# Performance work log

Hardware: AMD Instinct MI355X
Metric: run time of the kernel (lower is better)

The kernel has to match this reference:

```python
import jax, jax.numpy as jnp
import numpy as np


def setup_inputs() -> dict:
    key = jax.random.key(0)
    k1, k2 = jax.random.split(key)
    B, G, P = 64, 4999, 50
    raw_gene_expr = jax.random.normal(k1, (B, G), dtype=jnp.float32)
    # binary pathway membership matrix, mimics torch.randint(0, 2, (P, G)).float()
    pathway_gene_matrix = (jax.random.uniform(k2, (P, G)) < 0.5).astype(jnp.float32)
    return {"raw_gene_expr": raw_gene_expr, "pathway_gene_matrix": pathway_gene_matrix}


def reference(raw_gene_expr, pathway_gene_matrix):
    """Vectorized ssGSEA enrichment (compute_pathway_activations0).

    raw_gene_expr:        [B, G] float
    pathway_gene_matrix:  [P, G] binary float
    returns:              [B, P] signed max-deviation enrichment scores
    """
    B, G = raw_gene_expr.shape
    P = pathway_gene_matrix.shape[0]

    # Sort genes per sample in descending expression order
    order = jnp.argsort(-raw_gene_expr, axis=1)                      # [B, G]
    sorted_expr = jnp.take_along_axis(raw_gene_expr, order, axis=1)  # [B, G]

    # hit[b, p, i] = 1 if gene at sorted position i belongs to pathway p
    hit = (pathway_gene_matrix[:, order] > 0)                        # [P, B, G]
    hit = jnp.transpose(hit, (1, 0, 2)).astype(raw_gene_expr.dtype)  # [B, P, G]

    size = jnp.sum(pathway_gene_matrix > 0, axis=1).astype(raw_gene_expr.dtype)  # [P]

    # Weighted hit increments: |expr|^0.25 over hits, normalized per (sample, pathway)
    w = (jnp.abs(sorted_expr) ** 0.25)[:, None, :] * hit             # [B, P, G]
    s = jnp.sum(w, axis=-1, keepdims=True)
    w = jnp.where(s > 0, w / jnp.where(s > 0, s, 1.0), w)

    cum_hit = jnp.cumsum(w, axis=-1)                                 # [B, P, G]
    denom = jnp.maximum(G - size, 1.0)[None, :, None]                # guard size==G
    cum_miss = jnp.cumsum((1.0 - hit) / denom, axis=-1)              # [B, P, G]

    running = cum_hit - cum_miss                                     # [B, P, G]
    pos = jnp.argmax(jnp.abs(running), axis=-1)                      # [B, P]
    # signed max deviation == running value at the argmax of |running|
    es = jnp.take_along_axis(running, pos[..., None], axis=-1)[..., 0]  # [B, P]
    es = jnp.where(size[None, :] > 0, es, 0.0)
    return es
```

## Files before the change

kernel.cpp:

```cpp
#include <hip/hip_runtime.h>
#include <math.h>

typedef unsigned long long ull;

constexpr int Bc = 64;
constexpr int Gc = 4999;
constexpr int Pc = 50;

constexpr int RUN   = 1024;
constexpr int NRUN  = 5;
constexpr int NPAD  = NRUN * RUN;
constexpr int LPW   = 79;
constexpr ull PADKEY = 0xFFFFFFFFFFFFFFFFull;

__device__ __forceinline__ ull shfl_xor64(ull v, int lm) {
    int lo = __shfl_xor((int)(unsigned)(v & 0xFFFFFFFFull), lm, 64);
    int hi = __shfl_xor((int)(unsigned)(v >> 32), lm, 64);
    return ((ull)(unsigned)hi << 32) | (unsigned)lo;
}

__global__ __launch_bounds__(256) void chunk_sort(
    const float* __restrict__ expr, const float* __restrict__ pathway,
    ull* __restrict__ runs, ull* __restrict__ pbits, int P, int G)
{
    __shared__ ull key[RUN];
    const int r = blockIdx.x, b = blockIdx.y, tid = threadIdx.x;
    const int base = tid * 4;
    const float* row = expr + (size_t)b * G;

    ull v[4];
#pragma unroll
    for (int o = 0; o < 4; ++o) {
        int i = r * RUN + base + o;
        if (i < G) {
            unsigned u = __float_as_uint(row[i]);
            unsigned m = (u >> 31) ? ~u : (u | 0x80000000u);
            v[o] = ((ull)(~m) << 32) | (unsigned)i;
        } else {
            v[o] = PADKEY;
        }
    }

    for (int kk = 2; kk <= RUN; kk <<= 1) {
        const int j0 = kk >> 1;
        if (j0 >= 256) {
#pragma unroll
            for (int o = 0; o < 4; ++o) key[base + o] = v[o];
            __syncthreads();
            for (int j = j0; j >= 256; j >>= 1) {
#pragma unroll
                for (int t = tid; t < RUN / 2; t += 256) {
                    int i  = ((t & ~(j - 1)) << 1) | (t & (j - 1));
                    int ix = i | j;
                    ull a = key[i], c = key[ix];
                    bool up = ((i & kk) == 0);
                    if ((a > c) == up) { key[i] = c; key[ix] = a; }
                }
                __syncthreads();
            }
#pragma unroll
            for (int o = 0; o < 4; ++o) v[o] = key[base + o];
        }
        int jstart = (j0 > 128) ? 128 : j0;
        for (int j = jstart; j >= 4; j >>= 1) {
            int lm = j >> 2;
            bool takeMin = (((tid & lm) == 0) == ((base & kk) == 0));
#pragma unroll
            for (int o = 0; o < 4; ++o) {
                ull c = shfl_xor64(v[o], lm);
                ull mn = (v[o] < c) ? v[o] : c;
                ull mx = (v[o] < c) ? c : v[o];
                v[o] = takeMin ? mn : mx;
            }
        }
#pragma unroll
        for (int j = 2; j >= 1; j >>= 1) {
            if (j < kk) {
#pragma unroll
                for (int o = 0; o < 4; ++o) {
                    if ((o & j) == 0) {
                        bool up = (((base + o) & kk) == 0);
                        ull a = v[o], c = v[o | j];
                        if ((a > c) == up) { v[o] = c; v[o | j] = a; }
                    }
                }
            }
        }
    }

    ull* dst = runs + ((size_t)b * NRUN + r) * RUN;
#pragma unroll
    for (int o = 0; o < 4; ++o) dst[base + o] = v[o];

    if (r == 0) {
        int g = b * 256 + tid;
        if (g < G) {
            ull m = 0;
#pragma unroll
            for (int p = 0; p < Pc; ++p)
                if (pathway[(size_t)p * G + g] > 0.0f) m |= (1ull << p);
            pbits[g] = m;
        }
    }
}

__global__ __launch_bounds__(1024) void rank_scatter(
    const ull* __restrict__ runs,
    float* __restrict__ wqout, unsigned short* __restrict__ sidxout, int G)
{
    __shared__ ull runsLDS[NPAD];
    const int rg = blockIdx.x, b = blockIdx.y, tid = threadIdx.x;

    const ull* rowruns = runs + (size_t)b * NPAD;
    for (int i = tid; i < NPAD; i += 1024) runsLDS[i] = rowruns[i];
    __syncthreads();

    const int e = rg * 1024 + tid;
    const ull keyv = runsLDS[e];
    if (keyv == PADKEY) return;

    const int run = e >> 10;
    int rank = e & 1023;
#pragma unroll
    for (int rr = 0; rr < NRUN; ++rr) {
        if (rr == run) continue;
        const ull* arr = &runsLDS[rr * RUN];
        int pos = 0;
#pragma unroll
        for (int s = RUN; s >= 1; s >>= 1) {
            int np = pos + s;
            if (np <= RUN && arr[np - 1] < keyv) pos = np;
        }
        rank += pos;
    }

    int idx = (int)(unsigned)(keyv & 0xFFFFFFFFu);
    unsigned m = ~((unsigned)(keyv >> 32));
    unsigned absbits = ((m >> 31) ? m : ~m) & 0x7FFFFFFFu;
    float av = __uint_as_float(absbits);
    wqout[(size_t)b * G + rank] = sqrtf(sqrtf(av));
    sidxout[(size_t)b * G + rank] = (unsigned short)idx;
}

__global__ __launch_bounds__(256) void es_kernel(
    const float* __restrict__ wq, const unsigned short* __restrict__ sidx,
    const ull* __restrict__ pbits, float* __restrict__ out, int B, int P, int G)
{
    __shared__ float    swq[Gc];
    __shared__ unsigned sm32[Gc];

    const int pg = blockIdx.x;
    const int b  = blockIdx.y;
    const int tid = threadIdx.x;
    const int pbeg = pg * 13;
    const int pend = (pbeg + 13 < P) ? (pbeg + 13) : P;

    for (int i = tid; i < G; i += 256) {
        swq[i]  = wq[(size_t)b * G + i];
        sm32[i] = (unsigned)(pbits[sidx[(size_t)b * G + i]] >> pbeg);
    }
    __syncthreads();

    const int lane = tid & 63;
    const int w = tid >> 6;
    const int p0 = pbeg + w * 4;
    if (p0 >= pend) return;
    const int sh4 = w * 4;

    const int start = lane * LPW;
    const int cnt = (start + LPW < G) ? LPW : (G - start);

    double sw[4] = {0.0, 0.0, 0.0, 0.0};
    int sh[4] = {0, 0, 0, 0};
    for (int k = 0; k < cnt; ++k) {
        int s = start + k;
        unsigned nib = (sm32[s] >> sh4) & 15u;
        double wv = (double)swq[s];
#pragma unroll
        for (int q = 0; q < 4; ++q) {
            if ((nib >> q) & 1u) { sw[q] += wv; sh[q]++; }
        }
    }
    double norm[4], inv_denom[4], running[4];
    int sht[4];
#pragma unroll
    for (int q = 0; q < 4; ++q) {
        double swt = sw[q];
        int shq = sh[q];
#pragma unroll
        for (int off = 1; off < 64; off <<= 1) {
            swt += __shfl_xor(swt, off, 64);
            shq += __shfl_xor(shq, off, 64);
        }
        sht[q] = shq;
        norm[q]      = (swt > 0.0) ? 1.0 / swt : 1.0;
        inv_denom[q] = 1.0 / fmax((double)(G - shq), 1.0);
        double csum = sw[q] * norm[q] - (double)(cnt - sh[q]) * inv_denom[q];
        double x = csum;
#pragma unroll
        for (int off = 1; off < 64; off <<= 1) {
            double vv = __shfl_up(x, off, 64);
            if (lane >= off) x += vv;
        }
        running[q] = x - csum;
    }

    double bestv[4] = {-1.0, -1.0, -1.0, -1.0};
    double bestr[4] = {0.0, 0.0, 0.0, 0.0};
    int besti[4] = {0x7FFFFFFF, 0x7FFFFFFF, 0x7FFFFFFF, 0x7FFFFFFF};
    for (int k = 0; k < cnt; ++k) {
        int s = start + k;
        unsigned nib = (sm32[s] >> sh4) & 15u;
        double wv = (double)swq[s];
#pragma unroll
        for (int q = 0; q < 4; ++q) {
            running[q] += ((nib >> q) & 1u) ? wv * norm[q] : -inv_denom[q];
            double a = fabs(running[q]);
            if (a > bestv[q]) { bestv[q] = a; bestr[q] = running[q]; besti[q] = s; }
        }
    }
#pragma unroll
    for (int q = 0; q < 4; ++q) {
#pragma unroll
        for (int off = 1; off < 64; off <<= 1) {
            double ov  = __shfl_xor(bestv[q], off, 64);
            double orr = __shfl_xor(bestr[q], off, 64);
            int    oi  = __shfl_xor(besti[q], off, 64);
            if (ov > bestv[q] || (ov == bestv[q] && oi < besti[q])) {
                bestv[q] = ov; bestr[q] = orr; besti[q] = oi;
            }
        }
    }

    if (lane == 0) {
#pragma unroll
        for (int q = 0; q < 4; ++q) {
            int p = p0 + q;
            if (p < pend)
                out[(size_t)b * P + p] = (sht[q] > 0) ? (float)bestr[q] : 0.0f;
        }
    }
}

extern "C" void kernel_launch(void* const* d_in, const int* in_sizes, int n_in,
                              void* d_out, int out_size, void* d_ws, size_t ws_size,
                              hipStream_t stream) {
    const float* expr    = (const float*)d_in[0];
    const float* pathway = (const float*)d_in[1];
    float* out = (float*)d_out;

    char* ws = (char*)d_ws;
    ull*            pbits = (ull*)ws;
    ull*            runs  = (ull*)(ws + 40960);
    float*          wqa   = (float*)(ws + 2662400);
    unsigned short* sidx  = (unsigned short*)(ws + 3942144);

    chunk_sort<<<dim3(NRUN, Bc), dim3(256), 0, stream>>>(
        expr, pathway, runs, pbits, Pc, Gc);
    rank_scatter<<<dim3(NRUN, Bc), dim3(1024), 0, stream>>>(runs, wqa, sidx, Gc);
    es_kernel<<<dim3(4, Bc), dim3(256), 0, stream>>>(
        wqa, sidx, pbits, out, Bc, Pc, Gc);
}
```

Baseline: 111.0 us.

## Fuse sort, rank-scatter and enrichment into one cooperative kernel

Merges the three kernels into a single cooperative launch separated by grid-wide barriers, with a shared-memory union reused across stages. The rank stage now processes four elements per thread with 256-thread blocks, and the enrichment stage splits pathways into five groups of ten so each wave handles at most three. This removes inter-kernel launch gaps and adds parallelism in the scan stage, at the cost of grid-sync overhead and reduced thread count in the rank stage.

After: 210.0 us. +89.2%, slower.

```diff
diff --git a/kernel.cpp b/kernel.cpp
--- a/kernel.cpp
+++ b/kernel.cpp
@@ -1,6 +1,8 @@
 #include <hip/hip_runtime.h>
+#include <hip/hip_cooperative_groups.h>
 #include <math.h>
 
+namespace cg = cooperative_groups;
 typedef unsigned long long ull;
 
 constexpr int Bc = 64;
@@ -19,225 +21,231 @@
     return ((ull)(unsigned)hi << 32) | (unsigned)lo;
 }
 
-__global__ __launch_bounds__(256) void chunk_sort(
+__global__ __launch_bounds__(256) void fused_all(
     const float* __restrict__ expr, const float* __restrict__ pathway,
-    ull* __restrict__ runs, ull* __restrict__ pbits, int P, int G)
+    ull* __restrict__ pbits, ull* __restrict__ runs,
+    float* __restrict__ wq, unsigned short* __restrict__ sidx,
+    float* __restrict__ out)
 {
-    __shared__ ull key[RUN];
-    const int r = blockIdx.x, b = blockIdx.y, tid = threadIdx.x;
-    const int base = tid * 4;
-    const float* row = expr + (size_t)b * G;
-
-    ull v[4];
-#pragma unroll
-    for (int o = 0; o < 4; ++o) {
-        int i = r * RUN + base + o;
-        if (i < G) {
-            unsigned u = __float_as_uint(row[i]);
-            unsigned m = (u >> 31) ? ~u : (u | 0x80000000u);
-            v[o] = ((ull)(~m) << 32) | (unsigned)i;
-        } else {
-            v[o] = PADKEY;
+    __shared__ union {
+        ull key[RUN];
+        ull runsLDS[NPAD];
+        struct { float swq[Gc]; unsigned sm32[Gc]; } es;
+    } lds;
+
+    const int rg = blockIdx.x, b = blockIdx.y, tid = threadIdx.x;
+    const int G = Gc, P = Pc;
+    cg::grid_group grid = cg::this_grid();
+
+    {
+        const int base = tid * 4;
+        const float* row = expr + (size_t)b * G;
+        ull v[4];
+#pragma unroll
+        for (int o = 0; o < 4; ++o) {
+            int i = rg * RUN + base + o;
+            if (i < G) {
+                unsigned u = __float_as_uint(row[i]);
+                unsigned m = (u >> 31) ? ~u : (u | 0x80000000u);
+                v[o] = ((ull)(~m) << 32) | (unsigned)i;
+            } else {
+                v[o] = PADKEY;
+            }
+        }
+
+        for (int kk = 2; kk <= RUN; kk <<= 1) {
+            const int j0 = kk >> 1;
+            if (j0 >= 256) {
+#pragma unroll
+                for (int o = 0; o < 4; ++o) lds.key[base + o] = v[o];
+                __syncthreads();
+                for (int j = j0; j >= 256; j >>= 1) {
+#pragma unroll
+                    for (int t = tid; t < RUN / 2; t += 256) {
+                        int i  = ((t & ~(j - 1)) << 1) | (t & (j - 1));
+                        int ix = i | j;
+                        ull a = lds.key[i], c = lds.key[ix];
+                        bool up = ((i & kk) == 0);
+                        if ((a > c) == up) { lds.key[i] = c; lds.key[ix] = a; }
+                    }
+                    __syncthreads();
+                }
+#pragma unroll
+                for (int o = 0; o < 4; ++o) v[o] = lds.key[base + o];
+            }
+            int jstart = (j0 > 128) ? 128 : j0;
+            for (int j = jstart; j >= 4; j >>= 1) {
+                int lm = j >> 2;
+                bool takeMin = (((tid & lm) == 0) == ((base & kk) == 0));
+#pragma unroll
+                for (int o = 0; o < 4; ++o) {
+                    ull c = shfl_xor64(v[o], lm);
+                    ull mn = (v[o] < c) ? v[o] : c;
+                    ull mx = (v[o] < c) ? c : v[o];
+                    v[o] = takeMin ? mn : mx;
+                }
+            }
+#pragma unroll
+            for (int j = 2; j >= 1; j >>= 1) {
+                if (j < kk) {
+#pragma unroll
+                    for (int o = 0; o < 4; ++o) {
+                        if ((o & j) == 0) {
+                            bool up = (((base + o) & kk) == 0);
+                            ull a = v[o], c = v[o | j];
+                            if ((a > c) == up) { v[o] = c; v[o | j] = a; }
+                        }
+                    }
+                }
+            }
+        }
+
+        ull* dst = runs + ((size_t)b * NRUN + rg) * RUN;
+#pragma unroll
+        for (int o = 0; o < 4; ++o) dst[base + o] = v[o];
+
+        if (rg == 0) {
+            int g = b * 256 + tid;
+            if (g < G) {
+                ull m = 0;
+#pragma unroll
+                for (int p = 0; p < Pc; ++p)
+                    if (pathway[(size_t)p * G + g] > 0.0f) m |= (1ull << p);
+                pbits[g] = m;
+            }
         }
     }
 
-    for (int kk = 2; kk <= RUN; kk <<= 1) {
-        const int j0 = kk >> 1;
-        if (j0 >= 256) {
-#pragma unroll
-            for (int o = 0; o < 4; ++o) key[base + o] = v[o];
-            __syncthreads();
-            for (int j = j0; j >= 256; j >>= 1) {
-#pragma unroll
-                for (int t = tid; t < RUN / 2; t += 256) {
-                    int i  = ((t & ~(j - 1)) << 1) | (t & (j - 1));
-                    int ix = i | j;
-                    ull a = key[i], c = key[ix];
-                    bool up = ((i & kk) == 0);
-                    if ((a > c) == up) { key[i] = c; key[ix] = a; }
-                }
-                __syncthreads();
-            }
-#pragma unroll
-            for (int o = 0; o < 4; ++o) v[o] = key[base + o];
-        }
-        int jstart = (j0 > 128) ? 128 : j0;
-        for (int j = jstart; j >= 4; j >>= 1) {
-            int lm = j >> 2;
-            bool takeMin = (((tid & lm) == 0) == ((base & kk) == 0));
-#pragma unroll
-            for (int o = 0; o < 4; ++o) {
-                ull c = shfl_xor64(v[o], lm);
-                ull mn = (v[o] < c) ? v[o] : c;
-                ull mx = (v[o] < c) ? c : v[o];
-                v[o] = takeMin ? mn : mx;
-            }
-        }
-#pragma unroll
-        for (int j = 2; j >= 1; j >>= 1) {
-            if (j < kk) {
-#pragma unroll
-                for (int o = 0; o < 4; ++o) {
-                    if ((o & j) == 0) {
-                        bool up = (((base + o) & kk) == 0);
-                        ull a = v[o], c = v[o | j];
-                        if ((a > c) == up) { v[o] = c; v[o | j] = a; }
-                    }
-                }
-            }
+    grid.sync();
+    __syncthreads();
+
+    {
+        const ull* rowruns = runs + (size_t)b * NPAD;
+        for (int i = tid; i < NPAD; i += 256) lds.runsLDS[i] = rowruns[i];
+        __syncthreads();
+
+#pragma unroll
+        for (int o = 0; o < 4; ++o) {
+            const int e = rg * 1024 + o * 256 + tid;
+            const ull keyv = lds.runsLDS[e];
+            if (keyv == PADKEY) continue;
+            const int run = e >> 10;
+            int rank = e & 1023;
+#pragma unroll
+            for (int rr = 0; rr < NRUN; ++rr) {
+                if (rr == run) continue;
+                const ull* arr = &lds.runsLDS[rr * RUN];
+                int pos = 0;
+#pragma unroll
+                for (int s = RUN; s >= 1; s >>= 1) {
+                    int np = pos + s;
+                    if (np <= RUN && arr[np - 1] < keyv) pos = np;
+                }
+                rank += pos;
+            }
+            int idx = (int)(unsigned)(keyv & 0xFFFFFFFFu);
+            unsigned m = ~((unsigned)(keyv >> 32));
+            unsigned absbits = ((m >> 31) ? m : ~m) & 0x7FFFFFFFu;
+            float av = __uint_as_float(absbits);
+            wq[(size_t)b * G + rank] = sqrtf(sqrtf(av));
+            sidx[(size_t)b * G + rank] = (unsigned short)idx;
         }
     }
 
-    ull* dst = runs + ((size_t)b * NRUN + r) * RUN;
-#pragma unroll
-    for (int o = 0; o < 4; ++o) dst[base + o] = v[o];
-
-    if (r == 0) {
-        int g = b * 256 + tid;
-        if (g < G) {
-            ull m = 0;
-#pragma unroll
-            for (int p = 0; p < Pc; ++p)
-                if (pathway[(size_t)p * G + g] > 0.0f) m |= (1ull << p);
-            pbits[g] = m;
-        }
-    }
-}
-
-__global__ __launch_bounds__(1024) void rank_scatter(
-    const ull* __restrict__ runs,
-    float* __restrict__ wqout, unsigned short* __restrict__ sidxout, int G)
-{
-    __shared__ ull runsLDS[NPAD];
-    const int rg = blockIdx.x, b = blockIdx.y, tid = threadIdx.x;
-
-    const ull* rowruns = runs + (size_t)b * NPAD;
-    for (int i = tid; i < NPAD; i += 1024) runsLDS[i] = rowruns[i];
+    grid.sync();
     __syncthreads();
 
-    const int e = rg * 1024 + tid;
-    const ull keyv = runsLDS[e];
-    if (keyv == PADKEY) return;
-
-    const int run = e >> 10;
-    int rank = e & 1023;
-#pragma unroll
-    for (int rr = 0; rr < NRUN; ++rr) {
-        if (rr == run) continue;
-        const ull* arr = &runsLDS[rr * RUN];
-        int pos = 0;
-#pragma unroll
-        for (int s = RUN; s >= 1; s >>= 1) {
-            int np = pos + s;
-            if (np <= RUN && arr[np - 1] < keyv) pos = np;
-        }
-        rank += pos;
-    }
-
-    int idx = (int)(unsigned)(keyv & 0xFFFFFFFFu);
-    unsigned m = ~((unsigned)(keyv >> 32));
-    unsigned absbits = ((m >> 31) ? m : ~m) & 0x7FFFFFFFu;
-    float av = __uint_as_float(absbits);
-    wqout[(size_t)b * G + rank] = sqrtf(sqrtf(av));
-    sidxout[(size_t)b * G + rank] = (unsigned short)idx;
-}
-
-__global__ __launch_bounds__(256) void es_kernel(
-    const float* __restrict__ wq, const unsigned short* __restrict__ sidx,
-    const ull* __restrict__ pbits, float* __restrict__ out, int B, int P, int G)
-{
-    __shared__ float    swq[Gc];
-    __shared__ unsigned sm32[Gc];
-
-    const int pg = blockIdx.x;
-    const int b  = blockIdx.y;
-    const int tid = threadIdx.x;
-    const int pbeg = pg * 13;
-    const int pend = (pbeg + 13 < P) ? (pbeg + 13) : P;
-
-    for (int i = tid; i < G; i += 256) {
-        swq[i]  = wq[(size_t)b * G + i];
-        sm32[i] = (unsigned)(pbits[sidx[(size_t)b * G + i]] >> pbeg);
-    }
-    __syncthreads();
-
-    const int lane = tid & 63;
-    const int w = tid >> 6;
-    const int p0 = pbeg + w * 4;
-    if (p0 >= pend) return;
-    const int sh4 = w * 4;
-
-    const int start = lane * LPW;
-    const int cnt = (start + LPW < G) ? LPW : (G - start);
-
-    double sw[4] = {0.0, 0.0, 0.0, 0.0};
-    int sh[4] = {0, 0, 0, 0};
-    for (int k = 0; k < cnt; ++k) {
-        int s = start + k;
-        unsigned nib = (sm32[s] >> sh4) & 15u;
-        double wv = (double)swq[s];
-#pragma unroll
-        for (int q = 0; q < 4; ++q) {
-            if ((nib >> q) & 1u) { sw[q] += wv; sh[q]++; }
-        }
-    }
-    double norm[4], inv_denom[4], running[4];
-    int sht[4];
-#pragma unroll
-    for (int q = 0; q < 4; ++q) {
-        double swt = sw[q];
-        int shq = sh[q];
-#pragma unroll
-        for (int off = 1; off < 64; off <<= 1) {
-            swt += __shfl_xor(swt, off, 64);
-            shq += __shfl_xor(shq, off, 64);
-        }
-        sht[q] = shq;
-        norm[q]      = (swt > 0.0) ? 1.0 / swt : 1.0;
-        inv_denom[q] = 1.0 / fmax((double)(G - shq), 1.0);
-        double csum = sw[q] * norm[q] - (double)(cnt - sh[q]) * inv_denom[q];
-        double x = csum;
-#pragma unroll
-        for (int off = 1; off < 64; off <<= 1) {
-            double vv = __shfl_up(x, off, 64);
-            if (lane >= off) x += vv;
-        }
-        running[q] = x - csum;
-    }
-
-    double bestv[4] = {-1.0, -1.0, -1.0, -1.0};
-    double bestr[4] = {0.0, 0.0, 0.0, 0.0};
-    int besti[4] = {0x7FFFFFFF, 0x7FFFFFFF, 0x7FFFFFFF, 0x7FFFFFFF};
-    for (int k = 0; k < cnt; ++k) {
-        int s = start + k;
-        unsigned nib = (sm32[s] >> sh4) & 15u;
-        double wv = (double)swq[s];
-#pragma unroll
-        for (int q = 0; q < 4; ++q) {
-            running[q] += ((nib >> q) & 1u) ? wv * norm[q] : -inv_denom[q];
-            double a = fabs(running[q]);
-            if (a > bestv[q]) { bestv[q] = a; bestr[q] = running[q]; besti[q] = s; }
-        }
-    }
-#pragma unroll
-    for (int q = 0; q < 4; ++q) {
-#pragma unroll
-        for (int off = 1; off < 64; off <<= 1) {
-            double ov  = __shfl_xor(bestv[q], off, 64);
-            double orr = __shfl_xor(bestr[q], off, 64);
-            int    oi  = __shfl_xor(besti[q], off, 64);
-            if (ov > bestv[q] || (ov == bestv[q] && oi < besti[q])) {
-                bestv[q] = ov; bestr[q] = orr; besti[q] = oi;
-            }
-        }
-    }
-
-    if (lane == 0) {
-#pragma unroll
-        for (int q = 0; q < 4; ++q) {
-            int p = p0 + q;
-            if (p < pend)
-                out[(size_t)b * P + p] = (sht[q] > 0) ? (float)bestr[q] : 0.0f;
+    {
+        const int pg = rg;
+        const int pbeg = pg * 10;
+
+        for (int i = tid; i < G; i += 256) {
+            lds.es.swq[i]  = wq[(size_t)b * G + i];
+            lds.es.sm32[i] = (unsigned)(pbits[sidx[(size_t)b * G + i]] >> pbeg);
+        }
+        __syncthreads();
+
+        const int lane = tid & 63;
+        const int w = tid >> 6;
+        const int woff = (w == 0) ? 0 : (w == 1) ? 3 : (w == 2) ? 6 : 8;
+        const int np   = (w < 2) ? 3 : 2;
+        const int p0   = pbeg + woff;
+
+        const int start = lane * LPW;
+        const int cnt = (start + LPW < G) ? LPW : (G - start);
+
+        double sw[3] = {0.0, 0.0, 0.0};
+        int sh[3] = {0, 0, 0};
+        for (int k = 0; k < cnt; ++k) {
+            int s = start + k;
+            unsigned nib = (lds.es.sm32[s] >> woff) & 7u;
+            double wv = (double)lds.es.swq[s];
+#pragma unroll
+            for (int q = 0; q < 3; ++q) {
+                if (q < np && ((nib >> q) & 1u)) { sw[q] += wv; sh[q]++; }
+            }
+        }
+        double norm[3], inv_denom[3], running[3];
+        int sht[3];
+#pragma unroll
+        for (int q = 0; q < 3; ++q) {
+            double swt = sw[q];
+            int shq = sh[q];
+#pragma unroll
+            for (int off = 1; off < 64; off <<= 1) {
+                swt += __shfl_xor(swt, off, 64);
+                shq += __shfl_xor(shq, off, 64);
+            }
+            sht[q] = shq;
+            norm[q]      = (swt > 0.0) ? 1.0 / swt : 1.0;
+            inv_denom[q] = 1.0 / fmax((double)(G - shq), 1.0);
+            double csum = sw[q] * norm[q] - (double)(cnt - sh[q]) * inv_denom[q];
+            double x = csum;
+#pragma unroll
+            for (int off = 1; off < 64; off <<= 1) {
+                double vv = __shfl_up(x, off, 64);
+                if (lane >= off) x += vv;
+            }
+            running[q] = x - csum;
+        }
+
+        double bestv[3] = {-1.0, -1.0, -1.0};
+        double bestr[3] = {0.0, 0.0, 0.0};
+        int besti[3] = {0x7FFFFFFF, 0x7FFFFFFF, 0x7FFFFFFF};
+        for (int k = 0; k < cnt; ++k) {
+            int s = start + k;
+            unsigned nib = (lds.es.sm32[s] >> woff) & 7u;
+            double wv = (double)lds.es.swq[s];
+#pragma unroll
+            for (int q = 0; q < 3; ++q) {
+                if (q < np) {
+                    running[q] += ((nib >> q) & 1u) ? wv * norm[q] : -inv_denom[q];
+                    double a = fabs(running[q]);
+                    if (a > bestv[q]) { bestv[q] = a; bestr[q] = running[q]; besti[q] = s; }
+                }
+            }
+        }
+#pragma unroll
+        for (int q = 0; q < 3; ++q) {
+#pragma unroll
+            for (int off = 1; off < 64; off <<= 1) {
+                double ov  = __shfl_xor(bestv[q], off, 64);
+                double orr = __shfl_xor(bestr[q], off, 64);
+                int    oi  = __shfl_xor(besti[q], off, 64);
+                if (ov > bestv[q] || (ov == bestv[q] && oi < besti[q])) {
+                    bestv[q] = ov; bestr[q] = orr; besti[q] = oi;
+                }
+            }
+        }
+
+        if (lane == 0) {
+#pragma unroll
+            for (int q = 0; q < 3; ++q) {
+                if (q < np) {
+                    int p = p0 + q;
+                    out[(size_t)b * P + p] = (sht[q] > 0) ? (float)bestr[q] : 0.0f;
+                }
+            }
         }
     }
 }
@@ -255,9 +263,8 @@
     float*          wqa   = (float*)(ws + 2662400);
     unsigned short* sidx  = (unsigned short*)(ws + 3942144);
 
-    chunk_sort<<<dim3(NRUN, Bc), dim3(256), 0, stream>>>(
-        expr, pathway, runs, pbits, Pc, Gc);
-    rank_scatter<<<dim3(NRUN, Bc), dim3(1024), 0, stream>>>(runs, wqa, sidx, Gc);
-    es_kernel<<<dim3(4, Bc), dim3(256), 0, stream>>>(
-        wqa, sidx, pbits, out, Bc, Pc, Gc);
+    void* args[] = { (void*)&expr, (void*)&pathway, (void*)&pbits,
+                     (void*)&runs, (void*)&wqa, (void*)&sidx, (void*)&out };
+    hipLaunchCooperativeKernel((void*)fused_all, dim3(NRUN, Bc), dim3(256),
+                               args, 0, stream);
 }
```
